# Kernel optimization log

Hardware: AMD Instinct MI355X
Metric: run time of the kernel (lower is better)

The kernel has to match this reference:

```python
import jax, jax.numpy as jnp
import numpy as np

B, C, H, W = 8, 512, 64, 64
D = C // 8  # qk_downscale = 8


def setup_inputs() -> dict:
    key = jax.random.key(0)
    k1, k2, k3, k4, k5 = jax.random.split(key, 5)
    scale = 1.0 / np.sqrt(C)
    return {
        "x": jax.random.normal(k1, (B, C, H, W), dtype=jnp.float32),
        "Wq": jax.random.normal(k2, (D, C), dtype=jnp.float32) * scale,
        "Wk": jax.random.normal(k3, (D, C), dtype=jnp.float32) * scale,
        "Wv": jax.random.normal(k4, (C, C), dtype=jnp.float32) * scale,
        "gamma": jax.random.normal(k5, (1,), dtype=jnp.float32) * 0.1,
    }


def reference(x, Wq, Wk, Wv, gamma):
    b, c, h, w = x.shape
    n = h * w
    xf = x.reshape(b, c, n)                      # [B, C, N]
    # 1x1 Conv1d (bias=False) == channel matmul
    q = jnp.einsum('dc,bcn->bdn', Wq, xf)        # [B, D, N]
    k = jnp.einsum('dc,bcn->bdn', Wk, xf)        # [B, D, N]
    v = jnp.einsum('oc,bcn->bon', Wv, xf)        # [B, C, N]
    # torch.bmm(q.transpose(1,2), k) -> [B, N, N], unscaled
    qk = jnp.einsum('bdn,bdm->bnm', q, k)        # [B, N, N]
    # nn.Softmax(dim=1): normalize over the FIRST N axis (rows)
    attn = jax.nn.softmax(qk, axis=1)            # [B, N, N]
    # torch.bmm(v, qk_softmaxed) -> [B, C, N]
    out = gamma * jnp.einsum('bcn,bnm->bcm', v, attn) + xf
    return out.reshape(b, c, h, w)
```

## Files before the change

### kernel.cpp

```cpp
#include <hip/hip_runtime.h>
#include <math.h>
#include <stdint.h>

constexpr int Bn = 8;
constexpr int Cn = 512;
constexpr int Dn = 64;
constexpr int Nn = 4096;

typedef __bf16 bf16x8 __attribute__((ext_vector_type(8)));
typedef float  f32x16 __attribute__((ext_vector_type(16)));

typedef const __attribute__((address_space(1))) uint8_t* gptr_t;
typedef __attribute__((address_space(3))) uint8_t*       lptr_t;

static __device__ __forceinline__ uint32_t pkbf(float a, float b) {
    union { float f; uint32_t u; } x, y; x.f = a; y.f = b;
    uint32_t ra = (x.u + 0x7fffu + ((x.u >> 16) & 1u)) >> 16;
    uint32_t rb = (y.u + 0x7fffu + ((y.u >> 16) & 1u)) & 0xffff0000u;
    return ra | rb;
}

static __device__ __forceinline__ uint32_t cvt2(float a, float b) {
    union { __bf16 h[2]; uint32_t u; } p;
    p.h[0] = (__bf16)a; p.h[1] = (__bf16)b;
    return p.u;
}

static __device__ __forceinline__ float fexp2(float x) {
#if __has_builtin(__builtin_amdgcn_exp2f)
    return __builtin_amdgcn_exp2f(x);
#else
    return exp2f(x);
#endif
}

__global__ __launch_bounds__(256) void convert_w(
    const float* __restrict__ Wq, const float* __restrict__ Wk,
    const float* __restrict__ Wv, uint16_t* __restrict__ wb)
{
    int g = blockIdx.x * 256 + threadIdx.x;
    int tile = g >> 9;
    int s    = g & 511;
    int Ob = tile >> 3, cT = tile & 7;
    int ch = s >> 6,  o  = s & 63;
    const float* src;
    if (Ob == 0)       src = Wq + (size_t)o * Cn;
    else if (Ob == 1)  src = Wk + (size_t)o * Cn;
    else               src = Wv + (size_t)((Ob - 2) * 64 + o) * Cn;
    src += cT * 64 + ch * 8;
    float4 a = ((const float4*)src)[0];
    float4 c = ((const float4*)src)[1];
    uint4 u;
    u.x = pkbf(a.x, a.y); u.y = pkbf(a.z, a.w);
    u.z = pkbf(c.x, c.y); u.w = pkbf(c.z, c.w);
    *(uint4*)(wb + (size_t)g * 8) = u;
}

__global__ __launch_bounds__(256) void convert_x(
    const float* __restrict__ X, uint16_t* __restrict__ xt)
{
    __shared__ float Xs[64][68];
    const int ntile = blockIdx.x;
    const int cT    = blockIdx.y;
    const int b     = blockIdx.z;
    const int t  = threadIdx.x;
    const int lr = t >> 2;
    const int lc = (t & 3) << 4;
    const float* src = X + ((size_t)b * Cn + cT * 64 + lr) * Nn + ntile * 64 + lc;
    float4 v0 = ((const float4*)src)[0];
    float4 v1 = ((const float4*)src)[1];
    float4 v2 = ((const float4*)src)[2];
    float4 v3 = ((const float4*)src)[3];
    *(float4*)&Xs[lr][lc +  0] = v0;
    *(float4*)&Xs[lr][lc +  4] = v1;
    *(float4*)&Xs[lr][lc +  8] = v2;
    *(float4*)&Xs[lr][lc + 12] = v3;
    __syncthreads();
    const int nT = ntile >> 2, nb = ntile & 3;
    const size_t base = (((size_t)b * 16 + nT) * 8 + cT) * 8;
    #pragma unroll
    for (int ss = 0; ss < 2; ++ss) {
        int s  = t + ss * 256;
        int ch = s >> 6, nl = s & 63;
        uint4 u;
        u.x = pkbf(Xs[ch * 8 + 0][nl], Xs[ch * 8 + 1][nl]);
        u.y = pkbf(Xs[ch * 8 + 2][nl], Xs[ch * 8 + 3][nl]);
        u.z = pkbf(Xs[ch * 8 + 4][nl], Xs[ch * 8 + 5][nl]);
        u.w = pkbf(Xs[ch * 8 + 6][nl], Xs[ch * 8 + 7][nl]);
        *(uint4*)(xt + ((base + ch) * 256 + nb * 64 + nl) * 8) = u;
    }
}

__global__ __launch_bounds__(256, 2) void gemm_qkv(
    const uint16_t* __restrict__ wb, const uint16_t* __restrict__ xt,
    uint16_t* __restrict__ qt, uint16_t* __restrict__ kt,
    uint16_t* __restrict__ vt)
{
    __shared__ __align__(16) uint8_t Wlds[8192];
    __shared__ __align__(16) uint8_t Xlds[32768];
    const int nT = blockIdx.x;
    const int oB = blockIdx.y;
    const int b  = blockIdx.z;
    const int t    = threadIdx.x;
    const int lane = t & 63;
    const int wq   = __builtin_amdgcn_readfirstlane(t >> 6);
    const int mrow = lane & 31;
    const int qh   = lane >> 5;
    const uint8_t* wtiles = (const uint8_t*)wb + (size_t)oB * 8 * 8192;
    const uint8_t* xtiles = (const uint8_t*)xt + (((size_t)b * 16 + nT) * 8) * 32768;
    const bool isv = (oB >= 2);

    f32x16 acc[2][2];
    #pragma unroll
    for (int i = 0; i < 2; ++i)
        #pragma unroll
        for (int j = 0; j < 2; ++j)
            #pragma unroll
            for (int r = 0; r < 16; ++r) acc[i][j][r] = 0.f;

    for (int cT = 0; cT < 8; ++cT) {
        __syncthreads();
        #pragma unroll
        for (int i2 = 0; i2 < 2; ++i2) {
            int s = wq * 2 + i2;
            __builtin_amdgcn_global_load_lds(
                (gptr_t)(wtiles + cT * 8192 + s * 1024 + lane * 16),
                (lptr_t)(Wlds + s * 1024), 16, 0, 0);
        }
        #pragma unroll
        for (int i8 = 0; i8 < 8; ++i8) {
            int s = wq * 8 + i8;
            __builtin_amdgcn_global_load_lds(
                (gptr_t)(xtiles + cT * 32768 + s * 1024 + lane * 16),
                (lptr_t)(Xlds + s * 1024), 16, 0, 0);
        }
        __syncthreads();
        #pragma unroll
        for (int i = 0; i < 4; ++i) {
            int ch = 2 * i + qh;
            bf16x8 wf0 = *(const bf16x8*)(Wlds + ch * 1024 + mrow * 16);
            bf16x8 wf1 = *(const bf16x8*)(Wlds + ch * 1024 + (32 + mrow) * 16);
            bf16x8 xf0 = *(const bf16x8*)(Xlds + ch * 4096 + (wq * 64 + mrow) * 16);
            bf16x8 xf1 = *(const bf16x8*)(Xlds + ch * 4096 + (wq * 64 + 32 + mrow) * 16);
            if (!isv) {
                acc[0][0] = __builtin_amdgcn_mfma_f32_32x32x16_bf16(wf0, xf0, acc[0][0], 0, 0, 0);
                acc[0][1] = __builtin_amdgcn_mfma_f32_32x32x16_bf16(wf0, xf1, acc[0][1], 0, 0, 0);
                acc[1][0] = __builtin_amdgcn_mfma_f32_32x32x16_bf16(wf1, xf0, acc[1][0], 0, 0, 0);
                acc[1][1] = __builtin_amdgcn_mfma_f32_32x32x16_bf16(wf1, xf1, acc[1][1], 0, 0, 0);
            } else {
                acc[0][0] = __builtin_amdgcn_mfma_f32_32x32x16_bf16(xf0, wf0, acc[0][0], 0, 0, 0);
                acc[0][1] = __builtin_amdgcn_mfma_f32_32x32x16_bf16(xf0, wf1, acc[0][1], 0, 0, 0);
                acc[1][0] = __builtin_amdgcn_mfma_f32_32x32x16_bf16(xf1, wf0, acc[1][0], 0, 0, 0);
                acc[1][1] = __builtin_amdgcn_mfma_f32_32x32x16_bf16(xf1, wf1, acc[1][1], 0, 0, 0);
            }
        }
    }

    if (!isv) {
        uint16_t* dst = (oB == 0) ? qt : kt;
        const float qs = (oB == 0) ? 1.4426950408889634f : 1.0f;
        #pragma unroll
        for (int ot = 0; ot < 2; ++ot)
            #pragma unroll
            for (int ns = 0; ns < 2; ++ns) {
                int T = nT * 8 + wq * 2 + ns;
                size_t tb = ((size_t)b * 128 + T) * 2048;
                #pragma unroll
                for (int rr = 0; rr < 4; ++rr) {
                    uint2 u;
                    u.x = pkbf(qs * acc[ot][ns][4 * rr + 0], qs * acc[ot][ns][4 * rr + 1]);
                    u.y = pkbf(qs * acc[ot][ns][4 * rr + 2], qs * acc[ot][ns][4 * rr + 3]);
                    *(uint2*)(dst + tb + (size_t)(ot * 4 + rr) * 256 + mrow * 8 + 4 * qh) = u;
                }
            }
    } else {
        #pragma unroll
        for (int ns = 0; ns < 2; ++ns)
            #pragma unroll
            for (int ot = 0; ot < 2; ++ot) {
                int T = nT * 8 + wq * 2 + ns;
                int c_out = (oB - 2) * 64 + ot * 32 + mrow;
                size_t tb = ((size_t)b * 128 + T) * 16384;
                uint4 U0, U1;
                U0.x = pkbf(acc[ns][ot][ 0], acc[ns][ot][ 1]);
                U0.y = pkbf(acc[ns][ot][ 2], acc[ns][ot][ 3]);
                U0.z = pkbf(acc[ns][ot][ 4], acc[ns][ot][ 5]);
                U0.w = pkbf(acc[ns][ot][ 6], acc[ns][ot][ 7]);
                U1.x = pkbf(acc[ns][ot][ 8], acc[ns][ot][ 9]);
                U1.y = pkbf(acc[ns][ot][10], acc[ns][ot][11]);
                U1.z = pkbf(acc[ns][ot][12], acc[ns][ot][13]);
                U1.w = pkbf(acc[ns][ot][14], acc[ns][ot][15]);
                *(uint4*)(vt + tb + (size_t)qh      * 4096 + c_out * 8) = U0;
                *(uint4*)(vt + tb + (size_t)(2+qh)  * 4096 + c_out * 8) = U1;
            }
    }
}

__global__ __launch_bounds__(256, 2) void flash_attn(
    const uint16_t* __restrict__ qt, const uint16_t* __restrict__ kt,
    const uint16_t* __restrict__ vt, const float* __restrict__ X,
    const float* __restrict__ gamma, float* __restrict__ out)
{
    const int bid = blockIdx.x;
    const int x   = bid & 7;
    const int kk  = bid >> 3;
    const int mB  = kk & 15;
    const int grp = (kk >> 4) * 8 + x;
    const int b   = grp >> 2;
    const int cB  = grp & 3;

    const int t    = threadIdx.x;
    const int lane = t & 63;
    const int wq   = __builtin_amdgcn_readfirstlane(t >> 6);
    const int mrow = lane & 31;
    const int qh   = lane >> 5;

    const uint8_t* kbase = (const uint8_t*)kt + ((size_t)b * 128 + (size_t)mB * 8) * 4096;
    const uint8_t* vbase = (const uint8_t*)vt + (size_t)b * 128 * 32768
                           + (size_t)cB * 2048;
    const uint8_t* qbase = (const uint8_t*)qt + (size_t)b * 128 * 4096;

    bf16x8 kfr[2][4];
    #pragma unroll
    for (int mt = 0; mt < 2; ++mt)
        #pragma unroll
        for (int i = 0; i < 4; ++i)
            kfr[mt][i] = *(const bf16x8*)(kbase + (wq * 2 + mt) * 4096
                                          + (2 * i + qh) * 512 + mrow * 16);

    bf16x8 qcur[4];
    #pragma unroll
    for (int i = 0; i < 4; ++i)
        qcur[i] = *(const bf16x8*)(qbase + (2 * i + qh) * 512 + mrow * 16);

    f32x16 acc[2][4];
    #pragma unroll
    for (int mt = 0; mt < 2; ++mt)
        #pragma unroll
        for (int cf = 0; cf < 4; ++cf)
            #pragma unroll
            for (int r = 0; r < 16; ++r) acc[mt][cf][r] = 0.f;
    float lrun0 = 0.f, lrun1 = 0.f;

    constexpr float SBIAS = -86.5617024533378f;

    for (int T = 0; T < 128; ++T) {
        const uint8_t* vb_ = vbase + (size_t)T * 32768;
        bf16x8 vfA[4], vfC[4];
        #pragma unroll
        for (int cf = 0; cf < 4; ++cf) {
            int cloc = cf * 32 + mrow;
            vfA[cf] = *(const bf16x8*)(vb_ + (size_t)qh       * 8192 + cloc * 16);
            vfC[cf] = *(const bf16x8*)(vb_ + (size_t)(2 + qh) * 8192 + cloc * 16);
        }
        bf16x8 qnext[4];
        if (T < 127) {
            const uint8_t* qsrc = qbase + (size_t)(T + 1) * 4096;
            #pragma unroll
            for (int i = 0; i < 4; ++i)
                qnext[i] = *(const bf16x8*)(qsrc + (2 * i + qh) * 512 + mrow * 16);
        }

        f32x16 S0, S1;
        #pragma unroll
        for (int r = 0; r < 16; ++r) { S0[r] = SBIAS; S1[r] = SBIAS; }
        #pragma unroll
        for (int i = 0; i < 4; ++i) {
            S0 = __builtin_amdgcn_mfma_f32_32x32x16_bf16(qcur[i], kfr[0][i], S0, 0, 0, 0);
            S1 = __builtin_amdgcn_mfma_f32_32x32x16_bf16(qcur[i], kfr[1][i], S1, 0, 0, 0);
        }

        union pu { uint32_t u[4]; bf16x8 v; };
        pu Pf[2][2];
        {
            float p[16], ps = 0.f;
            #pragma unroll
            for (int r = 0; r < 16; ++r) { p[r] = fexp2(S0[r]); ps += p[r]; }
            lrun0 += ps;
            #pragma unroll
            for (int j = 0; j < 4; ++j) Pf[0][0].u[j] = cvt2(p[2 * j],     p[2 * j + 1]);
            #pragma unroll
            for (int j = 0; j < 4; ++j) Pf[0][1].u[j] = cvt2(p[8 + 2 * j], p[8 + 2 * j + 1]);
        }
        {
            float p[16], ps = 0.f;
            #pragma unroll
            for (int r = 0; r < 16; ++r) { p[r] = fexp2(S1[r]); ps += p[r]; }
            lrun1 += ps;
            #pragma unroll
            for (int j = 0; j < 4; ++j) Pf[1][0].u[j] = cvt2(p[2 * j],     p[2 * j + 1]);
            #pragma unroll
            for (int j = 0; j < 4; ++j) Pf[1][1].u[j] = cvt2(p[8 + 2 * j], p[8 + 2 * j + 1]);
        }

        #pragma unroll
        for (int cf = 0; cf < 4; ++cf) {
            #pragma unroll
            for (int mt = 0; mt < 2; ++mt) {
                acc[mt][cf] = __builtin_amdgcn_mfma_f32_32x32x16_bf16(vfA[cf], Pf[mt][0].v, acc[mt][cf], 0, 0, 0);
                acc[mt][cf] = __builtin_amdgcn_mfma_f32_32x32x16_bf16(vfC[cf], Pf[mt][1].v, acc[mt][cf], 0, 0, 0);
            }
        }

        #pragma unroll
        for (int i = 0; i < 4; ++i) qcur[i] = qnext[i];
    }

    float Lm[2];
    Lm[0] = lrun0 + __shfl_xor(lrun0, 32);
    Lm[1] = lrun1 + __shfl_xor(lrun1, 32);
    const float g   = gamma[0];
    const float* xb = X   + (size_t)b * Cn * Nn;
    float*       ob = out + (size_t)b * Cn * Nn;
    #pragma unroll
    for (int mt = 0; mt < 2; ++mt) {
        const float scale = g / Lm[mt];
        const int   m     = mB * 256 + wq * 64 + mt * 32 + mrow;
        #pragma unroll
        for (int cf = 0; cf < 4; ++cf)
            #pragma unroll
            for (int r = 0; r < 16; ++r) {
                int c = cB * 128 + cf * 32 + (r & 3) + 8 * (r >> 2) + 4 * qh;
                size_t idx = (size_t)c * Nn + m;
                ob[idx] = scale * acc[mt][cf][r] + xb[idx];
            }
    }
}

extern "C" void kernel_launch(void* const* d_in, const int* in_sizes, int n_in,
                              void* d_out, int out_size, void* d_ws, size_t ws_size,
                              hipStream_t stream)
{
    const float* x     = (const float*)d_in[0];
    const float* Wq    = (const float*)d_in[1];
    const float* Wk    = (const float*)d_in[2];
    const float* Wv    = (const float*)d_in[3];
    const float* gamma = (const float*)d_in[4];
    float* out = (float*)d_out;

    uint16_t* qt = (uint16_t*)d_ws;
    uint16_t* kt = qt + (size_t)2097152;
    uint16_t* vt = kt + (size_t)2097152;
    uint16_t* xt = vt + (size_t)16777216;
    uint16_t* wbuf = xt + (size_t)16777216;

    convert_w <<<dim3(160),       256, 0, stream>>>(Wq, Wk, Wv, wbuf);
    convert_x <<<dim3(64, 8, 8),  256, 0, stream>>>(x, xt);
    gemm_qkv  <<<dim3(16, 10, 8), 256, 0, stream>>>(wbuf, xt, qt, kt, vt);
    flash_attn<<<dim3(512),       256, 0, stream>>>(qt, kt, vt, x, gamma, out);
}
```

Before: 366.4 us.

## Double-buffer QKV GEMM LDS tiles and software-pipeline attention QK with PV

The QKV projection GEMM now double-buffers its W and X tiles in LDS, so the global-to-LDS load of the next channel tile is issued before computing on the current one, with one barrier per iteration instead of two. The attention loop is software-pipelined: the QK MFMAs for tile T are issued together with the PV MFMAs for tile T-1 at raised wave priority, and the V/Q loads and the exp/pack softmax work follow, with a final PV after the loop. The softmax row-sum is also split into four partial sums to shorten the dependency chain. This doubles LDS use in the GEMM, which may limit occupancy, and keeps more fragments live in registers in the attention kernel.

Result: slower. 457.1 us (+24.8%).

```diff
diff --git a/kernel.cpp b/kernel.cpp
--- a/kernel.cpp
+++ b/kernel.cpp
@@ -96,8 +96,8 @@
     uint16_t* __restrict__ qt, uint16_t* __restrict__ kt,
     uint16_t* __restrict__ vt)
 {
-    __shared__ __align__(16) uint8_t Wlds[8192];
-    __shared__ __align__(16) uint8_t Xlds[32768];
+    __shared__ __align__(16) uint8_t Wlds[2][8192];
+    __shared__ __align__(16) uint8_t Xlds[2][32768];
     const int nT = blockIdx.x;
     const int oB = blockIdx.y;
     const int b  = blockIdx.z;
@@ -118,30 +118,38 @@
             #pragma unroll
             for (int r = 0; r < 16; ++r) acc[i][j][r] = 0.f;
 
-    for (int cT = 0; cT < 8; ++cT) {
-        __syncthreads();
+    auto STAGE = [&](int bf, int cT) {
         #pragma unroll
         for (int i2 = 0; i2 < 2; ++i2) {
             int s = wq * 2 + i2;
             __builtin_amdgcn_global_load_lds(
                 (gptr_t)(wtiles + cT * 8192 + s * 1024 + lane * 16),
-                (lptr_t)(Wlds + s * 1024), 16, 0, 0);
+                (lptr_t)(Wlds[bf] + s * 1024), 16, 0, 0);
         }
         #pragma unroll
         for (int i8 = 0; i8 < 8; ++i8) {
             int s = wq * 8 + i8;
             __builtin_amdgcn_global_load_lds(
                 (gptr_t)(xtiles + cT * 32768 + s * 1024 + lane * 16),
-                (lptr_t)(Xlds + s * 1024), 16, 0, 0);
-        }
-        __syncthreads();
+                (lptr_t)(Xlds[bf] + s * 1024), 16, 0, 0);
+        }
+    };
+
+    STAGE(0, 0);
+    __syncthreads();
+
+    for (int cT = 0; cT < 8; ++cT) {
+        const int cur = cT & 1;
+        if (cT < 7) STAGE(cur ^ 1, cT + 1);
+        const uint8_t* Wb = Wlds[cur];
+        const uint8_t* Xb = Xlds[cur];
         #pragma unroll
         for (int i = 0; i < 4; ++i) {
             int ch = 2 * i + qh;
-            bf16x8 wf0 = *(const bf16x8*)(Wlds + ch * 1024 + mrow * 16);
-            bf16x8 wf1 = *(const bf16x8*)(Wlds + ch * 1024 + (32 + mrow) * 16);
-            bf16x8 xf0 = *(const bf16x8*)(Xlds + ch * 4096 + (wq * 64 + mrow) * 16);
-            bf16x8 xf1 = *(const bf16x8*)(Xlds + ch * 4096 + (wq * 64 + 32 + mrow) * 16);
+            bf16x8 wf0 = *(const bf16x8*)(Wb + ch * 1024 + mrow * 16);
+            bf16x8 wf1 = *(const bf16x8*)(Wb + ch * 1024 + (32 + mrow) * 16);
+            bf16x8 xf0 = *(const bf16x8*)(Xb + ch * 4096 + (wq * 64 + mrow) * 16);
+            bf16x8 xf1 = *(const bf16x8*)(Xb + ch * 4096 + (wq * 64 + 32 + mrow) * 16);
             if (!isv) {
                 acc[0][0] = __builtin_amdgcn_mfma_f32_32x32x16_bf16(wf0, xf0, acc[0][0], 0, 0, 0);
                 acc[0][1] = __builtin_amdgcn_mfma_f32_32x32x16_bf16(wf0, xf1, acc[0][1], 0, 0, 0);
@@ -154,6 +162,7 @@
                 acc[1][1] = __builtin_amdgcn_mfma_f32_32x32x16_bf16(xf1, wf1, acc[1][1], 0, 0, 0);
             }
         }
+        __syncthreads();
     }
 
     if (!isv) {
@@ -228,11 +237,6 @@
             kfr[mt][i] = *(const bf16x8*)(kbase + (wq * 2 + mt) * 4096
                                           + (2 * i + qh) * 512 + mrow * 16);
 
-    bf16x8 qcur[4];
-    #pragma unroll
-    for (int i = 0; i < 4; ++i)
-        qcur[i] = *(const bf16x8*)(qbase + (2 * i + qh) * 512 + mrow * 16);
-
     f32x16 acc[2][4];
     #pragma unroll
     for (int mt = 0; mt < 2; ++mt)
@@ -244,55 +248,36 @@
 
     constexpr float SBIAS = -86.5617024533378f;
 
-    for (int T = 0; T < 128; ++T) {
+    union pu { uint32_t u[4]; bf16x8 v; };
+    pu     Pf[2][2];
+    bf16x8 vfA[4], vfC[4];
+    bf16x8 qcur[4], qnext[4];
+
+    auto loadQ = [&](int T, bf16x8* dst) {
+        const uint8_t* qsrc = qbase + (size_t)T * 4096;
+        #pragma unroll
+        for (int i = 0; i < 4; ++i)
+            dst[i] = *(const bf16x8*)(qsrc + (2 * i + qh) * 512 + mrow * 16);
+    };
+    auto loadV = [&](int T) {
         const uint8_t* vb_ = vbase + (size_t)T * 32768;
-        bf16x8 vfA[4], vfC[4];
         #pragma unroll
         for (int cf = 0; cf < 4; ++cf) {
             int cloc = cf * 32 + mrow;
             vfA[cf] = *(const bf16x8*)(vb_ + (size_t)qh       * 8192 + cloc * 16);
             vfC[cf] = *(const bf16x8*)(vb_ + (size_t)(2 + qh) * 8192 + cloc * 16);
         }
-        bf16x8 qnext[4];
-        if (T < 127) {
-            const uint8_t* qsrc = qbase + (size_t)(T + 1) * 4096;
-            #pragma unroll
-            for (int i = 0; i < 4; ++i)
-                qnext[i] = *(const bf16x8*)(qsrc + (2 * i + qh) * 512 + mrow * 16);
-        }
-
-        f32x16 S0, S1;
-        #pragma unroll
-        for (int r = 0; r < 16; ++r) { S0[r] = SBIAS; S1[r] = SBIAS; }
+    };
+    auto qk = [&](f32x16& S0_, f32x16& S1_) {
+        #pragma unroll
+        for (int r = 0; r < 16; ++r) { S0_[r] = SBIAS; S1_[r] = SBIAS; }
         #pragma unroll
         for (int i = 0; i < 4; ++i) {
-            S0 = __builtin_amdgcn_mfma_f32_32x32x16_bf16(qcur[i], kfr[0][i], S0, 0, 0, 0);
-            S1 = __builtin_amdgcn_mfma_f32_32x32x16_bf16(qcur[i], kfr[1][i], S1, 0, 0, 0);
-        }
-
-        union pu { uint32_t u[4]; bf16x8 v; };
-        pu Pf[2][2];
-        {
-            float p[16], ps = 0.f;
-            #pragma unroll
-            for (int r = 0; r < 16; ++r) { p[r] = fexp2(S0[r]); ps += p[r]; }
-            lrun0 += ps;
-            #pragma unroll
-            for (int j = 0; j < 4; ++j) Pf[0][0].u[j] = cvt2(p[2 * j],     p[2 * j + 1]);
-            #pragma unroll
-            for (int j = 0; j < 4; ++j) Pf[0][1].u[j] = cvt2(p[8 + 2 * j], p[8 + 2 * j + 1]);
-        }
-        {
-            float p[16], ps = 0.f;
-            #pragma unroll
-            for (int r = 0; r < 16; ++r) { p[r] = fexp2(S1[r]); ps += p[r]; }
-            lrun1 += ps;
-            #pragma unroll
-            for (int j = 0; j < 4; ++j) Pf[1][0].u[j] = cvt2(p[2 * j],     p[2 * j + 1]);
-            #pragma unroll
-            for (int j = 0; j < 4; ++j) Pf[1][1].u[j] = cvt2(p[8 + 2 * j], p[8 + 2 * j + 1]);
-        }
-
+            S0_ = __builtin_amdgcn_mfma_f32_32x32x16_bf16(qcur[i], kfr[0][i], S0_, 0, 0, 0);
+            S1_ = __builtin_amdgcn_mfma_f32_32x32x16_bf16(qcur[i], kfr[1][i], S1_, 0, 0, 0);
+        }
+    };
+    auto pv = [&]() {
         #pragma unroll
         for (int cf = 0; cf < 4; ++cf) {
             #pragma unroll
@@ -301,10 +286,62 @@
                 acc[mt][cf] = __builtin_amdgcn_mfma_f32_32x32x16_bf16(vfC[cf], Pf[mt][1].v, acc[mt][cf], 0, 0, 0);
             }
         }
-
+    };
+    auto softmax_pack = [&](const f32x16& S0_, const f32x16& S1_) {
+        {
+            float p[16];
+            #pragma unroll
+            for (int r = 0; r < 16; ++r) p[r] = fexp2(S0_[r]);
+            float s0 = 0.f, s1 = 0.f, s2 = 0.f, s3 = 0.f;
+            #pragma unroll
+            for (int r = 0; r < 4; ++r) {
+                s0 += p[r]; s1 += p[4 + r]; s2 += p[8 + r]; s3 += p[12 + r];
+            }
+            lrun0 += (s0 + s1) + (s2 + s3);
+            #pragma unroll
+            for (int j = 0; j < 4; ++j) Pf[0][0].u[j] = cvt2(p[2 * j],     p[2 * j + 1]);
+            #pragma unroll
+            for (int j = 0; j < 4; ++j) Pf[0][1].u[j] = cvt2(p[8 + 2 * j], p[8 + 2 * j + 1]);
+        }
+        {
+            float p[16];
+            #pragma unroll
+            for (int r = 0; r < 16; ++r) p[r] = fexp2(S1_[r]);
+            float s0 = 0.f, s1 = 0.f, s2 = 0.f, s3 = 0.f;
+            #pragma unroll
+            for (int r = 0; r < 4; ++r) {
+                s0 += p[r]; s1 += p[4 + r]; s2 += p[8 + r]; s3 += p[12 + r];
+            }
+            lrun1 += (s0 + s1) + (s2 + s3);
+            #pragma unroll
+            for (int j = 0; j < 4; ++j) Pf[1][0].u[j] = cvt2(p[2 * j],     p[2 * j + 1]);
+            #pragma unroll
+            for (int j = 0; j < 4; ++j) Pf[1][1].u[j] = cvt2(p[8 + 2 * j], p[8 + 2 * j + 1]);
+        }
+    };
+
+    loadQ(0, qcur);
+    {
+        f32x16 S0, S1;
+        qk(S0, S1);
+        loadV(0);
+        loadQ(1, qnext);
+        softmax_pack(S0, S1);
+    }
+
+    for (int T = 1; T < 128; ++T) {
         #pragma unroll
         for (int i = 0; i < 4; ++i) qcur[i] = qnext[i];
-    }
+        __builtin_amdgcn_s_setprio(1);
+        f32x16 S0, S1;
+        qk(S0, S1);
+        pv();
+        __builtin_amdgcn_s_setprio(0);
+        loadV(T);
+        if (T < 127) loadQ(T + 1, qnext);
+        softmax_pack(S0, S1);
+    }
+    pv();
 
     float Lm[2];
     Lm[0] = lrun0 + __shfl_xor(lrun0, 32);
```

## Double-buffer QKV GEMM LDS and retile attention to cover all channels per block

Applied to the files above, without the earlier changes.

The QKV projection GEMM now double-buffers its W and X LDS tiles, so the next channel tile loads while the current one is multiplied, and one barrier per iteration replaces two. The attention kernel is retiled: each block covers 64 query columns across all 512 channels (two waves per 32 columns, each wave 256 channels) instead of 256 columns by 128 channels. This computes each QK^T and exp tile once per column instead of once per channel group, removing the 4x recompute of scores. In exchange each wave streams twice as many V fragments per step and holds 8 accumulators, which raises register pressure, and doubling LDS may reduce occupancy.

Result: faster. 358.6 us (-2.1%).

```diff
diff --git a/kernel.cpp b/kernel.cpp
--- a/kernel.cpp
+++ b/kernel.cpp
@@ -96,8 +96,8 @@
     uint16_t* __restrict__ qt, uint16_t* __restrict__ kt,
     uint16_t* __restrict__ vt)
 {
-    __shared__ __align__(16) uint8_t Wlds[8192];
-    __shared__ __align__(16) uint8_t Xlds[32768];
+    __shared__ __align__(16) uint8_t Wlds[2][8192];
+    __shared__ __align__(16) uint8_t Xlds[2][32768];
     const int nT = blockIdx.x;
     const int oB = blockIdx.y;
     const int b  = blockIdx.z;
@@ -118,30 +118,38 @@
             #pragma unroll
             for (int r = 0; r < 16; ++r) acc[i][j][r] = 0.f;
 
-    for (int cT = 0; cT < 8; ++cT) {
-        __syncthreads();
+    auto STAGE = [&](int bf, int cT) {
         #pragma unroll
         for (int i2 = 0; i2 < 2; ++i2) {
             int s = wq * 2 + i2;
             __builtin_amdgcn_global_load_lds(
                 (gptr_t)(wtiles + cT * 8192 + s * 1024 + lane * 16),
-                (lptr_t)(Wlds + s * 1024), 16, 0, 0);
+                (lptr_t)(Wlds[bf] + s * 1024), 16, 0, 0);
         }
         #pragma unroll
         for (int i8 = 0; i8 < 8; ++i8) {
             int s = wq * 8 + i8;
             __builtin_amdgcn_global_load_lds(
                 (gptr_t)(xtiles + cT * 32768 + s * 1024 + lane * 16),
-                (lptr_t)(Xlds + s * 1024), 16, 0, 0);
-        }
-        __syncthreads();
+                (lptr_t)(Xlds[bf] + s * 1024), 16, 0, 0);
+        }
+    };
+
+    STAGE(0, 0);
+    __syncthreads();
+
+    for (int cT = 0; cT < 8; ++cT) {
+        const int cur = cT & 1;
+        if (cT < 7) STAGE(cur ^ 1, cT + 1);
+        const uint8_t* Wb = Wlds[cur];
+        const uint8_t* Xb = Xlds[cur];
         #pragma unroll
         for (int i = 0; i < 4; ++i) {
             int ch = 2 * i + qh;
-            bf16x8 wf0 = *(const bf16x8*)(Wlds + ch * 1024 + mrow * 16);
-            bf16x8 wf1 = *(const bf16x8*)(Wlds + ch * 1024 + (32 + mrow) * 16);
-            bf16x8 xf0 = *(const bf16x8*)(Xlds + ch * 4096 + (wq * 64 + mrow) * 16);
-            bf16x8 xf1 = *(const bf16x8*)(Xlds + ch * 4096 + (wq * 64 + 32 + mrow) * 16);
+            bf16x8 wf0 = *(const bf16x8*)(Wb + ch * 1024 + mrow * 16);
+            bf16x8 wf1 = *(const bf16x8*)(Wb + ch * 1024 + (32 + mrow) * 16);
+            bf16x8 xf0 = *(const bf16x8*)(Xb + ch * 4096 + (wq * 64 + mrow) * 16);
+            bf16x8 xf1 = *(const bf16x8*)(Xb + ch * 4096 + (wq * 64 + 32 + mrow) * 16);
             if (!isv) {
                 acc[0][0] = __builtin_amdgcn_mfma_f32_32x32x16_bf16(wf0, xf0, acc[0][0], 0, 0, 0);
                 acc[0][1] = __builtin_amdgcn_mfma_f32_32x32x16_bf16(wf0, xf1, acc[0][1], 0, 0, 0);
@@ -154,6 +162,7 @@
                 acc[1][1] = __builtin_amdgcn_mfma_f32_32x32x16_bf16(xf1, wf1, acc[1][1], 0, 0, 0);
             }
         }
+        __syncthreads();
     }
 
     if (!isv) {
@@ -202,53 +211,47 @@
     const float* __restrict__ gamma, float* __restrict__ out)
 {
     const int bid = blockIdx.x;
-    const int x   = bid & 7;
-    const int kk  = bid >> 3;
-    const int mB  = kk & 15;
-    const int grp = (kk >> 4) * 8 + x;
-    const int b   = grp >> 2;
-    const int cB  = grp & 3;
+    const int b   = bid & 7;
+    const int mB  = bid >> 3;
 
     const int t    = threadIdx.x;
     const int lane = t & 63;
     const int wq   = __builtin_amdgcn_readfirstlane(t >> 6);
+    const int wm   = wq >> 1;
+    const int wc   = wq & 1;
     const int mrow = lane & 31;
     const int qh   = lane >> 5;
 
-    const uint8_t* kbase = (const uint8_t*)kt + ((size_t)b * 128 + (size_t)mB * 8) * 4096;
+    const uint8_t* kbase = (const uint8_t*)kt
+        + ((size_t)b * 128 + (size_t)mB * 2 + wm) * 4096;
     const uint8_t* vbase = (const uint8_t*)vt + (size_t)b * 128 * 32768
-                           + (size_t)cB * 2048;
+        + (size_t)wc * 4096;
     const uint8_t* qbase = (const uint8_t*)qt + (size_t)b * 128 * 4096;
 
-    bf16x8 kfr[2][4];
-    #pragma unroll
-    for (int mt = 0; mt < 2; ++mt)
-        #pragma unroll
-        for (int i = 0; i < 4; ++i)
-            kfr[mt][i] = *(const bf16x8*)(kbase + (wq * 2 + mt) * 4096
-                                          + (2 * i + qh) * 512 + mrow * 16);
+    bf16x8 kfr[4];
+    #pragma unroll
+    for (int i = 0; i < 4; ++i)
+        kfr[i] = *(const bf16x8*)(kbase + (2 * i + qh) * 512 + mrow * 16);
 
     bf16x8 qcur[4];
     #pragma unroll
     for (int i = 0; i < 4; ++i)
         qcur[i] = *(const bf16x8*)(qbase + (2 * i + qh) * 512 + mrow * 16);
 
-    f32x16 acc[2][4];
-    #pragma unroll
-    for (int mt = 0; mt < 2; ++mt)
-        #pragma unroll
-        for (int cf = 0; cf < 4; ++cf)
-            #pragma unroll
-            for (int r = 0; r < 16; ++r) acc[mt][cf][r] = 0.f;
-    float lrun0 = 0.f, lrun1 = 0.f;
+    f32x16 acc[8];
+    #pragma unroll
+    for (int cf = 0; cf < 8; ++cf)
+        #pragma unroll
+        for (int r = 0; r < 16; ++r) acc[cf][r] = 0.f;
+    float lrun = 0.f;
 
     constexpr float SBIAS = -86.5617024533378f;
 
     for (int T = 0; T < 128; ++T) {
         const uint8_t* vb_ = vbase + (size_t)T * 32768;
-        bf16x8 vfA[4], vfC[4];
-        #pragma unroll
-        for (int cf = 0; cf < 4; ++cf) {
+        bf16x8 vfA[8], vfC[8];
+        #pragma unroll
+        for (int cf = 0; cf < 8; ++cf) {
             int cloc = cf * 32 + mrow;
             vfA[cf] = *(const bf16x8*)(vb_ + (size_t)qh       * 8192 + cloc * 16);
             vfC[cf] = *(const bf16x8*)(vb_ + (size_t)(2 + qh) * 8192 + cloc * 16);
@@ -261,70 +264,55 @@
                 qnext[i] = *(const bf16x8*)(qsrc + (2 * i + qh) * 512 + mrow * 16);
         }
 
-        f32x16 S0, S1;
-        #pragma unroll
-        for (int r = 0; r < 16; ++r) { S0[r] = SBIAS; S1[r] = SBIAS; }
-        #pragma unroll
-        for (int i = 0; i < 4; ++i) {
-            S0 = __builtin_amdgcn_mfma_f32_32x32x16_bf16(qcur[i], kfr[0][i], S0, 0, 0, 0);
-            S1 = __builtin_amdgcn_mfma_f32_32x32x16_bf16(qcur[i], kfr[1][i], S1, 0, 0, 0);
-        }
+        f32x16 S;
+        #pragma unroll
+        for (int r = 0; r < 16; ++r) S[r] = SBIAS;
+        #pragma unroll
+        for (int i = 0; i < 4; ++i)
+            S = __builtin_amdgcn_mfma_f32_32x32x16_bf16(qcur[i], kfr[i], S, 0, 0, 0);
 
         union pu { uint32_t u[4]; bf16x8 v; };
-        pu Pf[2][2];
+        pu Pf0, Pf1;
         {
-            float p[16], ps = 0.f;
-            #pragma unroll
-            for (int r = 0; r < 16; ++r) { p[r] = fexp2(S0[r]); ps += p[r]; }
-            lrun0 += ps;
-            #pragma unroll
-            for (int j = 0; j < 4; ++j) Pf[0][0].u[j] = cvt2(p[2 * j],     p[2 * j + 1]);
-            #pragma unroll
-            for (int j = 0; j < 4; ++j) Pf[0][1].u[j] = cvt2(p[8 + 2 * j], p[8 + 2 * j + 1]);
-        }
-        {
-            float p[16], ps = 0.f;
-            #pragma unroll
-            for (int r = 0; r < 16; ++r) { p[r] = fexp2(S1[r]); ps += p[r]; }
-            lrun1 += ps;
-            #pragma unroll
-            for (int j = 0; j < 4; ++j) Pf[1][0].u[j] = cvt2(p[2 * j],     p[2 * j + 1]);
-            #pragma unroll
-            for (int j = 0; j < 4; ++j) Pf[1][1].u[j] = cvt2(p[8 + 2 * j], p[8 + 2 * j + 1]);
-        }
-
-        #pragma unroll
-        for (int cf = 0; cf < 4; ++cf) {
-            #pragma unroll
-            for (int mt = 0; mt < 2; ++mt) {
-                acc[mt][cf] = __builtin_amdgcn_mfma_f32_32x32x16_bf16(vfA[cf], Pf[mt][0].v, acc[mt][cf], 0, 0, 0);
-                acc[mt][cf] = __builtin_amdgcn_mfma_f32_32x32x16_bf16(vfC[cf], Pf[mt][1].v, acc[mt][cf], 0, 0, 0);
+            float p[16];
+            #pragma unroll
+            for (int r = 0; r < 16; ++r) p[r] = fexp2(S[r]);
+            float s0 = 0.f, s1 = 0.f, s2 = 0.f, s3 = 0.f;
+            #pragma unroll
+            for (int r = 0; r < 4; ++r) {
+                s0 += p[r]; s1 += p[4 + r]; s2 += p[8 + r]; s3 += p[12 + r];
             }
+            lrun += (s0 + s1) + (s2 + s3);
+            #pragma unroll
+            for (int j = 0; j < 4; ++j) Pf0.u[j] = cvt2(p[2 * j],     p[2 * j + 1]);
+            #pragma unroll
+            for (int j = 0; j < 4; ++j) Pf1.u[j] = cvt2(p[8 + 2 * j], p[8 + 2 * j + 1]);
+        }
+
+        #pragma unroll
+        for (int cf = 0; cf < 8; ++cf) {
+            acc[cf] = __builtin_amdgcn_mfma_f32_32x32x16_bf16(vfA[cf], Pf0.v, acc[cf], 0, 0, 0);
+            acc[cf] = __builtin_amdgcn_mfma_f32_32x32x16_bf16(vfC[cf], Pf1.v, acc[cf], 0, 0, 0);
         }
 
         #pragma unroll
         for (int i = 0; i < 4; ++i) qcur[i] = qnext[i];
     }
 
-    float Lm[2];
-    Lm[0] = lrun0 + __shfl_xor(lrun0, 32);
-    Lm[1] = lrun1 + __shfl_xor(lrun1, 32);
+    const float Lm  = lrun + __shfl_xor(lrun, 32);
     const float g   = gamma[0];
+    const float scale = g / Lm;
     const float* xb = X   + (size_t)b * Cn * Nn;
     float*       ob = out + (size_t)b * Cn * Nn;
-    #pragma unroll
-    for (int mt = 0; mt < 2; ++mt) {
-        const float scale = g / Lm[mt];
-        const int   m     = mB * 256 + wq * 64 + mt * 32 + mrow;
-        #pragma unroll
-        for (int cf = 0; cf < 4; ++cf)
-            #pragma unroll
-            for (int r = 0; r < 16; ++r) {
-                int c = cB * 128 + cf * 32 + (r & 3) + 8 * (r >> 2) + 4 * qh;
-                size_t idx = (size_t)c * Nn + m;
-                ob[idx] = scale * acc[mt][cf][r] + xb[idx];
-            }
-    }
+    const int m = mB * 64 + wm * 32 + mrow;
+    #pragma unroll
+    for (int cf = 0; cf < 8; ++cf)
+        #pragma unroll
+        for (int r = 0; r < 16; ++r) {
+            int c = wc * 256 + cf * 32 + (r & 3) + 8 * (r >> 2) + 4 * qh;
+            size_t idx = (size_t)c * Nn + m;
+            ob[idx] = scale * acc[cf][r] + xb[idx];
+        }
 }
 
 extern "C" void kernel_launch(void* const* d_in, const int* in_sizes, int n_in,
```
